# Kernel tuning notes

Measured on AMD Instinct MI355X. Metric: run time of the kernel, lower is better.

## Reference

```python
import jax, jax.numpy as jnp
import numpy as np

CONTEXT_LENGTHS = [1, 3, 5, 7]
PADS = [(f - 1) // 2 for f in CONTEXT_LENGTHS]  # p(f) for odd f
B, H, L, DK = 2, 8, 1024, 64
C = H * DK  # conv channels = d_k * n_heads


def _conv1d(x, w, b, pad):
    # x: (b, C, L), w: (C, C, f), b: (C,) -- torch Conv1d semantics
    y = jax.lax.conv_general_dilated(
        x, w, window_strides=(1,), padding=[(pad, pad)],
        dimension_numbers=("NCH", "OIH", "NCH"))
    return y + b[None, :, None]


def _plane(a, w, b, pad, out_len):
    # Faithful to: conv(a.reshape(b, h*d_k, -1)).reshape(b, h, -1, d_k)[:, :, :out_len, :]
    bsz, h, l, d = a.shape
    y = _conv1d(a.reshape(bsz, h * d, l), w, b, pad)
    return y.reshape(bsz, h, -1, d)[:, :, :out_len, :]


def setup_inputs() -> dict:
    key = jax.random.key(0)
    ks = jax.random.split(key, 12)
    inp = {
        "Q": jax.random.normal(ks[0], (B, H, L, DK), jnp.float32),
        "K": jax.random.normal(ks[1], (B, H, L, DK), jnp.float32),
        "V": jax.random.normal(ks[2], (B, H, L, DK), jnp.float32),
        # causal mask: True = masked
        "attn_mask": jnp.broadcast_to(
            jnp.triu(jnp.ones((L, L), jnp.bool_), k=1), (B, H, L, L)),
    }
    for i, f in enumerate(CONTEXT_LENGTHS):
        scale = 1.0 / np.sqrt(C * f)
        inp[f"conv_w{i}"] = jax.random.normal(ks[3 + i], (C, C, f), jnp.float32) * scale
        inp[f"conv_b{i}"] = jax.random.normal(ks[7 + i], (C,), jnp.float32) * scale
    return inp


def reference(Q, K, V, attn_mask,
              conv_w0, conv_b0, conv_w1, conv_b1,
              conv_w2, conv_b2, conv_w3, conv_b3):
    ws = [conv_w0, conv_w1, conv_w2, conv_w3]
    bs = [conv_b0, conv_b1, conv_b2, conv_b3]
    b, h, l, d_k = Q.shape
    l_k = K.shape[2]
    p = len(CONTEXT_LENGTHS)
    Q_l = [_plane(Q, ws[i], bs[i], PADS[i], l) for i in range(p)]
    K_l = [_plane(K, ws[i], bs[i], PADS[i], l_k) for i in range(p)]
    # replicate torch.cat(dim=0).reshape(b, h, p, l, d) exactly (row-major)
    Q_p = jnp.concatenate(Q_l, axis=0).reshape(b, h, p, l, d_k)
    K_p = jnp.concatenate(K_l, axis=0).reshape(b, h, p, l_k, d_k)
    scores = jnp.einsum("bhpqd,bhpkd->bhpqk", Q_p, K_p) / np.sqrt(d_k).astype(np.float32)
    scores = jnp.where(attn_mask[:, :, None, :, :], jnp.float32(-1e9), scores)
    attn = jax.nn.softmax(scores, axis=-1)
    attn = jnp.max(attn, axis=2)  # max over planes -> (b,h,q,k)
    context = jnp.einsum("bhqk,bhkd->bhqd", attn, V)
    return (context, attn)
```

## Files before the change

kernel.cpp:

```cpp
#include <hip/hip_runtime.h>
#include <math.h>

#define C_CH 512
#define L_SEQ 1024
#define DK 64
#define NP 4
#define SC2 0.1803368801111f

typedef __attribute__((ext_vector_type(8))) short short8;
typedef __attribute__((ext_vector_type(4))) float f32x4;

__device__ __forceinline__ unsigned short f2bf(float f) {
    union { float f; unsigned u; } v; v.f = f;
    unsigned u = v.u;
    u += 0x7FFFu + ((u >> 16) & 1u);
    return (unsigned short)(u >> 16);
}

__device__ __forceinline__ void unpack_group(int G, int& qt, int& kt0, int& kt1,
                                             int& j, int& ng) {
    int q = 15, cum = 0, jj = 0;
    for (; q >= 0; q--) {
        int g = (q + 4) >> 2;
        if (G < cum + g) { jj = G - cum; break; }
        cum += g;
    }
    qt = q;
    ng = (q + 4) >> 2;
    j = jj;
    int n = q + 1;
    kt0 = (jj * n) / ng;
    kt1 = ((jj + 1) * n) / ng;
}

__global__ __launch_bounds__(256)
void prep_w_kernel(const float* __restrict__ w0, const float* __restrict__ w1,
                   const float* __restrict__ w2, const float* __restrict__ w3,
                   unsigned short* __restrict__ Wb) {
    int tg = blockIdx.y;
    int plane, t;
    if (tg < 1)      { plane = 0; t = tg; }
    else if (tg < 4) { plane = 1; t = tg - 1; }
    else if (tg < 9) { plane = 2; t = tg - 4; }
    else             { plane = 3; t = tg - 9; }
    const float* W = (plane == 0) ? w0 : (plane == 1) ? w1 : (plane == 2) ? w2 : w3;
    const int f = (plane == 0) ? 1 : (plane == 1) ? 3 : (plane == 2) ? 5 : 7;

    int co = blockIdx.x * 32 + (threadIdx.x >> 3);
    int c8 = threadIdx.x & 7;
    for (int it = 0; it < 8; it++) {
        int ci = c8 * 8 + it * 64;
        unsigned short o[8];
#pragma unroll
        for (int jj = 0; jj < 8; jj++)
            o[jj] = f2bf(W[(size_t)(co * C_CH + ci + jj) * f + t]);
        *(short8*)&Wb[((size_t)tg * C_CH + co) * C_CH + ci] = *(short8*)o;
    }
}

__global__ __launch_bounds__(256)
void prep_x_kernel(const float* __restrict__ Qin, const float* __restrict__ Kin,
                   unsigned short* __restrict__ Xt) {
    int tb = blockIdx.z;
    int tensor = tb >> 1, b = tb & 1;
    const float* X = (tensor ? Kin : Qin) + (size_t)b * C_CH * L_SEQ;
    unsigned short* O = Xt + (size_t)tb * 1032 * C_CH;

    int pos0 = blockIdx.x * 64;
    int ci0  = blockIdx.y * 64;
    int tid = threadIdx.x;

    __shared__ float tile[64][65];
    int tx = tid & 15, ty = tid >> 4;
#pragma unroll
    for (int rr = 0; rr < 4; rr++) {
        int ci_l = ty + rr * 16;
        float4 v = *(const float4*)&X[(size_t)(ci0 + ci_l) * L_SEQ + pos0 + tx * 4];
        tile[tx * 4 + 0][ci_l] = v.x;
        tile[tx * 4 + 1][ci_l] = v.y;
        tile[tx * 4 + 2][ci_l] = v.z;
        tile[tx * 4 + 3][ci_l] = v.w;
    }
    __syncthreads();
#pragma unroll
    for (int pp = 0; pp < 2; pp++) {
        int pos_l = (tid >> 3) + pp * 32;
        int cg = (tid & 7) * 8;
        unsigned short o[8];
#pragma unroll
        for (int jj = 0; jj < 8; jj++) o[jj] = f2bf(tile[pos_l][cg + jj]);
        *(short8*)&O[(size_t)(pos0 + pos_l + 4) * C_CH + ci0 + cg] = *(short8*)o;
    }
    if (blockIdx.x == 0) {
        int r = tid >> 6, cc = tid & 63;
        O[(size_t)r * C_CH + ci0 + cc] = 0;
    }
    if (blockIdx.x == 15) {
        int r = tid >> 6, cc = tid & 63;
        O[(size_t)(1028 + r) * C_CH + ci0 + cc] = 0;
    }
}

__global__ __launch_bounds__(256)
void conv_mfma_kernel(const unsigned short* __restrict__ Xt,
                      const unsigned short* __restrict__ Wb,
                      const float* __restrict__ b0, const float* __restrict__ b1,
                      const float* __restrict__ b2, const float* __restrict__ b3,
                      unsigned short* __restrict__ Qp, unsigned short* __restrict__ Kp) {
    const int fs[4]   = {1, 3, 5, 7};
    const int toff[4] = {0, 1, 4, 9};
    int id = blockIdx.x;
    int plane, rel;
    if (id < 128)      { plane = 0; rel = id; }
    else if (id < 256) { plane = 1; rel = id - 128; }
    else if (id < 384) { plane = 3; rel = id - 256; }
    else               { plane = 2; rel = id - 384; }
    int co0  = (rel & 3) * 128;
    int pos0 = ((rel >> 2) & 7) * 128;
    int tb   = rel >> 5;
    int tensor = tb >> 1, b = tb & 1;
    const int f   = fs[plane];
    const int pad = (f - 1) >> 1;
    const int n   = f * 16;
    const float* bias = (plane == 0) ? b0 : (plane == 1) ? b1 : (plane == 2) ? b2 : b3;
    unsigned short* Out = tensor ? Kp : Qp;
    const unsigned short* Xbase = Xt + (size_t)tb * 1032 * C_CH;

    __shared__ __align__(16) unsigned short As[2][4096];
    __shared__ __align__(16) unsigned short Bs[2][4096];

    int tid  = threadIdx.x;
    int w    = tid >> 6;
    int lane = tid & 63;
    int l15  = lane & 15;
    int quad = lane >> 4;
    int wm = (w & 1) * 64;
    int wn = (w >> 1) * 64;
    int rowL = tid >> 2;
    int cS   = tid & 3;

    int woff[2];
#pragma unroll
    for (int rep = 0; rep < 2; rep++) {
        int r = rowL + rep * 64;
        int line = r >> 1;
        int sl = (((r & 1) << 2) | cS) ^ (line & 7);
        woff[rep] = line * 64 + sl * 8;
    }
    int aoff[4], boff[4];
#pragma unroll
    for (int mi = 0; mi < 4; mi++) {
        int r = wm + mi * 16 + l15;
        int line = r >> 1;
        aoff[mi] = line * 64 + ((((r & 1) << 2) | quad) ^ (line & 7)) * 8;
        int r2 = wn + mi * 16 + l15;
        int line2 = r2 >> 1;
        boff[mi] = line2 * 64 + ((((r2 & 1) << 2) | quad) ^ (line2 & 7)) * 8;
    }

    f32x4 acc[4][4];
#pragma unroll
    for (int mi = 0; mi < 4; mi++)
#pragma unroll
        for (int ni = 0; ni < 4; ni++) acc[mi][ni] = (f32x4){0.f, 0.f, 0.f, 0.f};

    short8 pA[2], pB[2];
    {
        const unsigned short* Wsl = Wb + ((size_t)toff[plane] * C_CH + co0) * C_CH;
        const unsigned short* Xsl = Xbase + (size_t)(pos0 - pad + 4) * C_CH;
#pragma unroll
        for (int rep = 0; rep < 2; rep++) {
            int r = rowL + rep * 64;
            pA[rep] = *(const short8*)&Wsl[(size_t)r * C_CH + cS * 8];
            pB[rep] = *(const short8*)&Xsl[(size_t)r * C_CH + cS * 8];
        }
    }

    for (int it = 0; it < n; it++) {
        int cur = it & 1;
        *(short8*)&As[cur][woff[0]] = pA[0];
        *(short8*)&As[cur][woff[1]] = pA[1];
        *(short8*)&Bs[cur][woff[0]] = pB[0];
        *(short8*)&Bs[cur][woff[1]] = pB[1];
        __syncthreads();

        if (it + 1 < n) {
            int t = (it + 1) >> 4, cc = (it + 1) & 15;
            const unsigned short* Wsl =
                Wb + ((size_t)(toff[plane] + t) * C_CH + co0) * C_CH + cc * 32;
            const unsigned short* Xsl =
                Xbase + (size_t)(pos0 + t - pad + 4) * C_CH + cc * 32;
#pragma unroll
            for (int rep = 0; rep < 2; rep++) {
                int r = rowL + rep * 64;
                pA[rep] = *(const short8*)&Wsl[(size_t)r * C_CH + cS * 8];
                pB[rep] = *(const short8*)&Xsl[(size_t)r * C_CH + cS * 8];
            }
        }

        short8 af[4], bf[4];
#pragma unroll
        for (int mi = 0; mi < 4; mi++) af[mi] = *(const short8*)&As[cur][aoff[mi]];
#pragma unroll
        for (int ni = 0; ni < 4; ni++) bf[ni] = *(const short8*)&Bs[cur][boff[ni]];
#pragma unroll
        for (int mi = 0; mi < 4; mi++)
#pragma unroll
            for (int ni = 0; ni < 4; ni++)
                acc[mi][ni] = __builtin_amdgcn_mfma_f32_16x16x32_bf16(
                    af[mi], bf[ni], acc[mi][ni], 0, 0, 0);
    }

#pragma unroll
    for (int mi = 0; mi < 4; mi++)
#pragma unroll
        for (int r = 0; r < 4; r++) {
            int co = co0 + wm + mi * 16 + quad * 4 + r;
            int h = co >> 6, cl = co & 63;
            float bv = bias[co];
            size_t sbase = (size_t)((b * 8 + h) * NP + plane) * L_SEQ * DK;
#pragma unroll
            for (int ni = 0; ni < 4; ni++) {
                int pos = pos0 + wn + ni * 16 + l15;
                int l = cl * 16 + (pos >> 6);
                int d = pos & 63;
                Out[sbase + (size_t)l * DK + d] = f2bf(acc[mi][ni][r] + bv);
            }
        }
}

__global__ __launch_bounds__(256)
void attn_stats_kernel(const unsigned short* __restrict__ Qb,
                       const unsigned short* __restrict__ Kb,
                       float* __restrict__ pl) {
    int qt, kt0, kt1, j, ng;
    unpack_group(blockIdx.x, qt, kt0, kt1, j, ng);
    int bh = blockIdx.y;
    int tid = threadIdx.x;
    int q0 = qt * 64;

    int b2 = bh >> 3, h2 = bh & 7;
    int plane  = b2 * 2 + (h2 >> 2);
    int b_orig = (h2 >> 1) & 1;
    int h_base = (h2 & 1) * 4;
    int w = tid >> 6, lane = tid & 63, l15 = lane & 15, quad = lane >> 4;

    const unsigned short* kbase[NP];
    short8 qa[NP][2];
#pragma unroll
    for (int p = 0; p < NP; p++) {
        size_t slice = (size_t)((b_orig * 8 + h_base + p) * NP + plane);
        kbase[p] = Kb + slice * L_SEQ * DK;
        const unsigned short* qrow =
            Qb + (slice * L_SEQ + (size_t)(q0 + w * 16 + l15)) * DK + quad * 8;
        qa[p][0] = *(const short8*)(qrow);
        qa[p][1] = *(const short8*)(qrow + 32);
    }

    float l[NP][4];
#pragma unroll
    for (int p = 0; p < NP; p++)
        for (int r = 0; r < 4; r++) l[p][r] = 0.f;

    for (int kt = kt0; kt < kt1; kt++) {
        int k0 = kt * 64;
        bool diag = (kt == qt);
#pragma unroll
        for (int p = 0; p < NP; p++) {
            f32x4 c[4];
#pragma unroll
            for (int s = 0; s < 4; s++) {
                const unsigned short* kr =
                    kbase[p] + (size_t)(k0 + s * 16 + l15) * DK + quad * 8;
                short8 kb0 = *(const short8*)(kr);
                short8 kb1 = *(const short8*)(kr + 32);
                f32x4 acc = {0.f, 0.f, 0.f, 0.f};
                acc = __builtin_amdgcn_mfma_f32_16x16x32_bf16(qa[p][0], kb0, acc, 0, 0, 0);
                acc = __builtin_amdgcn_mfma_f32_16x16x32_bf16(qa[p][1], kb1, acc, 0, 0, 0);
                c[s] = acc;
            }
#pragma unroll
            for (int r = 0; r < 4; r++) {
                int row_local = quad * 4 + r + w * 16;
#pragma unroll
                for (int s = 0; s < 4; s++) {
                    float x = c[s][r] * SC2;
                    if (diag && (s * 16 + l15 > row_local)) x = -1e30f;
                    l[p][r] += exp2f(x);
                }
            }
        }
    }

    size_t base = ((size_t)(bh * 16 + qt) * 4 + j) * 256;
#pragma unroll
    for (int p = 0; p < NP; p++)
#pragma unroll
        for (int r = 0; r < 4; r++) {
            float ll = l[p][r];
            ll += __shfl_xor(ll, 1);
            ll += __shfl_xor(ll, 2);
            ll += __shfl_xor(ll, 4);
            ll += __shfl_xor(ll, 8);
            if (l15 == 0)
                pl[base + p * 64 + (w * 16 + quad * 4 + r)] = ll;
        }
}

__global__ __launch_bounds__(256)
void attn_combine_kernel(const float* __restrict__ pl,
                         float* __restrict__ fstats,
                         float* __restrict__ out_attn) {
    int qt = blockIdx.x, bh = blockIdx.y;
    int tid = threadIdx.x;
    int ng = (qt + 4) >> 2;
    size_t sb = (size_t)(bh * 16 + qt) * 4 * 256;

    float l = 0.f;
    for (int g = 0; g < ng; g++)
        l += pl[sb + (size_t)g * 256 + tid];
    fstats[(size_t)(bh * 16 + qt) * 256 + tid] = __log2f(l);

    int r = tid >> 2;
    float4 z = make_float4(0.f, 0.f, 0.f, 0.f);
    int kz = (qt + 1) * 64;
    size_t abase = ((size_t)bh * L_SEQ + qt * 64 + r) * L_SEQ;
    for (int k = kz + (tid & 3) * 4; k < L_SEQ; k += 16)
        *(float4*)&out_attn[abase + k] = z;
}

__global__ __launch_bounds__(256)
void attn_apply_kernel(const unsigned short* __restrict__ Qb,
                       const unsigned short* __restrict__ Kb,
                       const float* __restrict__ V,
                       const float* __restrict__ fstats,
                       float* __restrict__ pctx, float* __restrict__ out_attn) {
    int qt, kt0, kt1, j, ng;
    unpack_group(blockIdx.x, qt, kt0, kt1, j, ng);
    int bh = blockIdx.y;
    int tid = threadIdx.x;
    int q0 = qt * 64;

    int b2 = bh >> 3, h2 = bh & 7;
    int plane  = b2 * 2 + (h2 >> 2);
    int b_orig = (h2 >> 1) & 1;
    int h_base = (h2 & 1) * 4;
    int w = tid >> 6, lane = tid & 63, l15 = lane & 15, quad = lane >> 4;

    __shared__ float zsm[NP * 64];
    __shared__ __align__(16) unsigned short ast[64 * 80];
    __shared__ __align__(16) unsigned short vts[2][64 * 80];

    zsm[tid] = fstats[(size_t)(bh * 16 + qt) * 256 + tid];

    const unsigned short* kbase[NP];
    short8 qa[NP][2];
#pragma unroll
    for (int p = 0; p < NP; p++) {
        size_t slice = (size_t)((b_orig * 8 + h_base + p) * NP + plane);
        kbase[p] = Kb + slice * L_SEQ * DK;
        const unsigned short* qrow =
            Qb + (slice * L_SEQ + (size_t)(q0 + w * 16 + l15)) * DK + quad * 8;
        qa[p][0] = *(const short8*)(qrow);
        qa[p][1] = *(const short8*)(qrow + 32);
    }

    f32x4 ctxc[4];
#pragma unroll
    for (int ds = 0; ds < 4; ds++) ctxc[ds] = (f32x4){0.f, 0.f, 0.f, 0.f};

    for (int kt = kt0; kt < kt1; kt++) {
        int k0 = kt * 64;
        bool diag = (kt == qt);
        unsigned short* vb = vts[kt & 1];

        {
            int kl = tid >> 2, db = (tid & 3) * 16;
            const float* vr = V + ((size_t)bh * L_SEQ + k0 + kl) * DK + db;
            float vv[16];
            *(float4*)&vv[0]  = *(const float4*)(vr);
            *(float4*)&vv[4]  = *(const float4*)(vr + 4);
            *(float4*)&vv[8]  = *(const float4*)(vr + 8);
            *(float4*)&vv[12] = *(const float4*)(vr + 12);
#pragma unroll
            for (int jj = 0; jj < 16; jj++)
                vb[(db + jj) * 80 + kl] = f2bf(vv[jj]);
        }
        __syncthreads();

        float run[4][4];
#pragma unroll
        for (int s = 0; s < 4; s++)
            for (int r = 0; r < 4; r++) run[s][r] = -1e30f;

#pragma unroll
        for (int p = 0; p < NP; p++) {
            f32x4 c[4];
#pragma unroll
            for (int s = 0; s < 4; s++) {
                const unsigned short* kr =
                    kbase[p] + (size_t)(k0 + s * 16 + l15) * DK + quad * 8;
                short8 kb0 = *(const short8*)(kr);
                short8 kb1 = *(const short8*)(kr + 32);
                f32x4 acc = {0.f, 0.f, 0.f, 0.f};
                acc = __builtin_amdgcn_mfma_f32_16x16x32_bf16(qa[p][0], kb0, acc, 0, 0, 0);
                acc = __builtin_amdgcn_mfma_f32_16x16x32_bf16(qa[p][1], kb1, acc, 0, 0, 0);
                c[s] = acc;
            }
#pragma unroll
            for (int r = 0; r < 4; r++) {
                float zp = zsm[p * 64 + (quad * 4 + r + w * 16)];
#pragma unroll
                for (int s = 0; s < 4; s++)
                    run[s][r] = fmaxf(run[s][r], c[s][r] * SC2 - zp);
            }
        }

#pragma unroll
        for (int s = 0; s < 4; s++)
#pragma unroll
            for (int r = 0; r < 4; r++) {
                int qloc = w * 16 + quad * 4 + r;
                bool masked = diag && (s * 16 + l15 > qloc);
                float a = masked ? 0.f : exp2f(run[s][r]);
                out_attn[((size_t)bh * L_SEQ + q0 + qloc) * L_SEQ + k0 + s * 16 + l15] = a;
                ast[qloc * 80 + s * 16 + l15] = f2bf(a);
            }

        short8 af0 = *(const short8*)&ast[(w * 16 + l15) * 80 + quad * 8];
        short8 af1 = *(const short8*)&ast[(w * 16 + l15) * 80 + 32 + quad * 8];
#pragma unroll
        for (int ds = 0; ds < 4; ds++) {
            short8 bf0 = *(const short8*)&vb[(ds * 16 + l15) * 80 + quad * 8];
            short8 bf1 = *(const short8*)&vb[(ds * 16 + l15) * 80 + 32 + quad * 8];
            ctxc[ds] = __builtin_amdgcn_mfma_f32_16x16x32_bf16(af0, bf0, ctxc[ds], 0, 0, 0);
            ctxc[ds] = __builtin_amdgcn_mfma_f32_16x16x32_bf16(af1, bf1, ctxc[ds], 0, 0, 0);
        }
    }

    size_t pbase = ((size_t)(bh * 16 + qt) * 4 + j) * 4096;
#pragma unroll
    for (int ds = 0; ds < 4; ds++)
#pragma unroll
        for (int r = 0; r < 4; r++) {
            int qloc = w * 16 + quad * 4 + r;
            pctx[pbase + (size_t)qloc * 64 + ds * 16 + l15] = ctxc[ds][r];
        }
}

__global__ __launch_bounds__(256)
void ctx_reduce_kernel(const float* __restrict__ pctx, float* __restrict__ out_ctx) {
    int qt = blockIdx.x, bh = blockIdx.y;
    int tid = threadIdx.x;
    int ng = (qt + 4) >> 2;
    size_t base = (size_t)(bh * 16 + qt) * 4 * 4096;
    int row = tid >> 2, c = (tid & 3) * 16;
    size_t off = (size_t)row * 64 + c;

    float4 a0 = *(const float4*)&pctx[base + off];
    float4 a1 = *(const float4*)&pctx[base + off + 4];
    float4 a2 = *(const float4*)&pctx[base + off + 8];
    float4 a3 = *(const float4*)&pctx[base + off + 12];
    for (int g = 1; g < ng; g++) {
        size_t gb = base + (size_t)g * 4096 + off;
        float4 b0 = *(const float4*)&pctx[gb];
        float4 b1 = *(const float4*)&pctx[gb + 4];
        float4 b2 = *(const float4*)&pctx[gb + 8];
        float4 b3 = *(const float4*)&pctx[gb + 12];
        a0.x += b0.x; a0.y += b0.y; a0.z += b0.z; a0.w += b0.w;
        a1.x += b1.x; a1.y += b1.y; a1.z += b1.z; a1.w += b1.w;
        a2.x += b2.x; a2.y += b2.y; a2.z += b2.z; a2.w += b2.w;
        a3.x += b3.x; a3.y += b3.y; a3.z += b3.z; a3.w += b3.w;
    }
    size_t ob = ((size_t)bh * L_SEQ + qt * 64 + row) * DK + c;
    *(float4*)&out_ctx[ob]      = a0;
    *(float4*)&out_ctx[ob + 4]  = a1;
    *(float4*)&out_ctx[ob + 8]  = a2;
    *(float4*)&out_ctx[ob + 12] = a3;
}

extern "C" void kernel_launch(void* const* d_in, const int* in_sizes, int n_in,
                              void* d_out, int out_size, void* d_ws, size_t ws_size,
                              hipStream_t stream) {
    const float* Q  = (const float*)d_in[0];
    const float* K  = (const float*)d_in[1];
    const float* V  = (const float*)d_in[2];
    const float* w0 = (const float*)d_in[4];
    const float* b0 = (const float*)d_in[5];
    const float* w1 = (const float*)d_in[6];
    const float* b1 = (const float*)d_in[7];
    const float* w2 = (const float*)d_in[8];
    const float* b2 = (const float*)d_in[9];
    const float* w3 = (const float*)d_in[10];
    const float* b3 = (const float*)d_in[11];

    char* ws = (char*)d_ws;
    unsigned short* Wb = (unsigned short*)(ws);
    unsigned short* Xt = (unsigned short*)(ws + 8388608);
    unsigned short* Qp = (unsigned short*)(ws + 12615680);
    unsigned short* Kp = (unsigned short*)(ws + 21004288);
    float* pctx        = (float*)(ws + 29392896);
    float* pl     = (float*)(ws + 8388608);
    float* fstats = (float*)(ws + 8388608 + 1048576);

    float* out_ctx  = (float*)d_out;
    float* out_attn = out_ctx + 1048576;

    prep_w_kernel<<<dim3(16, 16), 256, 0, stream>>>(w0, w1, w2, w3, Wb);
    prep_x_kernel<<<dim3(16, 8, 4), 256, 0, stream>>>(Q, K, Xt);
    conv_mfma_kernel<<<dim3(512), 256, 0, stream>>>(Xt, Wb, b0, b1, b2, b3, Qp, Kp);
    attn_stats_kernel<<<dim3(40, 16), 256, 0, stream>>>(Qp, Kp, pl);
    attn_combine_kernel<<<dim3(16, 16), 256, 0, stream>>>(pl, fstats, out_attn);
    attn_apply_kernel<<<dim3(40, 16), 256, 0, stream>>>(Qp, Kp, V, fstats,
                                                        pctx, out_attn);
    ctx_reduce_kernel<<<dim3(16, 16), 256, 0, stream>>>(pctx, out_ctx);
}
```

Baseline: 355.4 us.

## Halve conv tile width, stage output via LDS, fold combine kernel into neighbors

The conv GEMM tile shrinks from 128x128 to 128x64 positions, doubling the grid to 1024 blocks for better CU fill. The epilogue is staged through shared memory so each thread writes 16-byte coalesced rows instead of scattered 2-byte stores. The separate combine kernel is removed: the stats kernel gets extra blocks that zero the masked part of the attention output, and the apply kernel sums the partial row sums and takes the log itself. This saves one launch and more parallelism in exchange for less reuse per conv tile and some redundant reductions.

```diff
diff --git a/kernel.cpp b/kernel.cpp
--- a/kernel.cpp
+++ b/kernel.cpp
@@ -110,14 +110,11 @@
     const int fs[4]   = {1, 3, 5, 7};
     const int toff[4] = {0, 1, 4, 9};
     int id = blockIdx.x;
-    int plane, rel;
-    if (id < 128)      { plane = 0; rel = id; }
-    else if (id < 256) { plane = 1; rel = id - 128; }
-    else if (id < 384) { plane = 3; rel = id - 256; }
-    else               { plane = 2; rel = id - 384; }
+    int plane = (id < 256) ? 0 : (id < 512) ? 1 : (id < 768) ? 3 : 2;
+    int rel = id & 255;
     int co0  = (rel & 3) * 128;
-    int pos0 = ((rel >> 2) & 7) * 128;
-    int tb   = rel >> 5;
+    int pos0 = ((rel >> 2) & 15) * 64;
+    int tb   = rel >> 6;
     int tensor = tb >> 1, b = tb & 1;
     const int f   = fs[plane];
     const int pad = (f - 1) >> 1;
@@ -127,7 +124,7 @@
     const unsigned short* Xbase = Xt + (size_t)tb * 1032 * C_CH;
 
     __shared__ __align__(16) unsigned short As[2][4096];
-    __shared__ __align__(16) unsigned short Bs[2][4096];
+    __shared__ __align__(16) unsigned short Bs[2][2048];
 
     int tid  = threadIdx.x;
     int w    = tid >> 6;
@@ -135,53 +132,54 @@
     int l15  = lane & 15;
     int quad = lane >> 4;
     int wm = (w & 1) * 64;
-    int wn = (w >> 1) * 64;
-    int rowL = tid >> 2;
-    int cS   = tid & 3;
-
-    int woff[2];
+    int wn = (w >> 1) * 32;
+
+    int rA0 = tid >> 2, sA = tid & 3;
+    int woffA[2], woffB;
 #pragma unroll
     for (int rep = 0; rep < 2; rep++) {
-        int r = rowL + rep * 64;
+        int r = rA0 + rep * 64;
         int line = r >> 1;
-        int sl = (((r & 1) << 2) | cS) ^ (line & 7);
-        woff[rep] = line * 64 + sl * 8;
-    }
-    int aoff[4], boff[4];
+        woffA[rep] = line * 64 + (((((r & 1) << 2) | sA)) ^ (line & 7)) * 8;
+    }
+    {
+        int line = rA0 >> 1;
+        woffB = line * 64 + (((((rA0 & 1) << 2) | sA)) ^ (line & 7)) * 8;
+    }
+    int aoff[4], boff[2];
 #pragma unroll
     for (int mi = 0; mi < 4; mi++) {
         int r = wm + mi * 16 + l15;
         int line = r >> 1;
         aoff[mi] = line * 64 + ((((r & 1) << 2) | quad) ^ (line & 7)) * 8;
-        int r2 = wn + mi * 16 + l15;
-        int line2 = r2 >> 1;
-        boff[mi] = line2 * 64 + ((((r2 & 1) << 2) | quad) ^ (line2 & 7)) * 8;
-    }
-
-    f32x4 acc[4][4];
+    }
+#pragma unroll
+    for (int ni = 0; ni < 2; ni++) {
+        int r = wn + ni * 16 + l15;
+        int line = r >> 1;
+        boff[ni] = line * 64 + ((((r & 1) << 2) | quad) ^ (line & 7)) * 8;
+    }
+
+    f32x4 acc[4][2];
 #pragma unroll
     for (int mi = 0; mi < 4; mi++)
 #pragma unroll
-        for (int ni = 0; ni < 4; ni++) acc[mi][ni] = (f32x4){0.f, 0.f, 0.f, 0.f};
-
-    short8 pA[2], pB[2];
+        for (int ni = 0; ni < 2; ni++) acc[mi][ni] = (f32x4){0.f, 0.f, 0.f, 0.f};
+
+    short8 pA[2], pB;
     {
         const unsigned short* Wsl = Wb + ((size_t)toff[plane] * C_CH + co0) * C_CH;
         const unsigned short* Xsl = Xbase + (size_t)(pos0 - pad + 4) * C_CH;
-#pragma unroll
-        for (int rep = 0; rep < 2; rep++) {
-            int r = rowL + rep * 64;
-            pA[rep] = *(const short8*)&Wsl[(size_t)r * C_CH + cS * 8];
-            pB[rep] = *(const short8*)&Xsl[(size_t)r * C_CH + cS * 8];
-        }
+        pA[0] = *(const short8*)&Wsl[(size_t)rA0 * C_CH + sA * 8];
+        pA[1] = *(const short8*)&Wsl[(size_t)(rA0 + 64) * C_CH + sA * 8];
+        pB    = *(const short8*)&Xsl[(size_t)rA0 * C_CH + sA * 8];
     }
 
     for (int it = 0; it < n; it++) {
         int cur = it & 1;
-        *(short8*)&As[cur][woff[0]] = pA[0];
-        *(short8*)&As[cur][woff[1]] = pA[1];
-        *(short8*)&Bs[cur][woff[0]] = pB[0];
-        *(short8*)&Bs[cur][woff[1]] = pB[1];
+        *(short8*)&As[cur][woffA[0]] = pA[0];
+        *(short8*)&As[cur][woffA[1]] = pA[1];
+        *(short8*)&Bs[cur][woffB]    = pB;
         __syncthreads();
 
         if (it + 1 < n) {
@@ -190,53 +188,76 @@
                 Wb + ((size_t)(toff[plane] + t) * C_CH + co0) * C_CH + cc * 32;
             const unsigned short* Xsl =
                 Xbase + (size_t)(pos0 + t - pad + 4) * C_CH + cc * 32;
-#pragma unroll
-            for (int rep = 0; rep < 2; rep++) {
-                int r = rowL + rep * 64;
-                pA[rep] = *(const short8*)&Wsl[(size_t)r * C_CH + cS * 8];
-                pB[rep] = *(const short8*)&Xsl[(size_t)r * C_CH + cS * 8];
-            }
-        }
-
-        short8 af[4], bf[4];
+            pA[0] = *(const short8*)&Wsl[(size_t)rA0 * C_CH + sA * 8];
+            pA[1] = *(const short8*)&Wsl[(size_t)(rA0 + 64) * C_CH + sA * 8];
+            pB    = *(const short8*)&Xsl[(size_t)rA0 * C_CH + sA * 8];
+        }
+
+        short8 af[4], bf[2];
 #pragma unroll
         for (int mi = 0; mi < 4; mi++) af[mi] = *(const short8*)&As[cur][aoff[mi]];
 #pragma unroll
-        for (int ni = 0; ni < 4; ni++) bf[ni] = *(const short8*)&Bs[cur][boff[ni]];
+        for (int ni = 0; ni < 2; ni++) bf[ni] = *(const short8*)&Bs[cur][boff[ni]];
 #pragma unroll
         for (int mi = 0; mi < 4; mi++)
 #pragma unroll
-            for (int ni = 0; ni < 4; ni++)
+            for (int ni = 0; ni < 2; ni++)
                 acc[mi][ni] = __builtin_amdgcn_mfma_f32_16x16x32_bf16(
                     af[mi], bf[ni], acc[mi][ni], 0, 0, 0);
     }
 
+    __syncthreads();
+    unsigned short* Cs = &As[0][0];
 #pragma unroll
     for (int mi = 0; mi < 4; mi++)
 #pragma unroll
         for (int r = 0; r < 4; r++) {
-            int co = co0 + wm + mi * 16 + quad * 4 + r;
-            int h = co >> 6, cl = co & 63;
-            float bv = bias[co];
-            size_t sbase = (size_t)((b * 8 + h) * NP + plane) * L_SEQ * DK;
-#pragma unroll
-            for (int ni = 0; ni < 4; ni++) {
-                int pos = pos0 + wn + ni * 16 + l15;
-                int l = cl * 16 + (pos >> 6);
-                int d = pos & 63;
-                Out[sbase + (size_t)l * DK + d] = f2bf(acc[mi][ni][r] + bv);
-            }
-        }
+            int co_l = wm + mi * 16 + quad * 4 + r;
+            float bv = bias[co0 + co_l];
+#pragma unroll
+            for (int ni = 0; ni < 2; ni++)
+                Cs[co_l * 64 + wn + ni * 16 + l15] = f2bf(acc[mi][ni][r] + bv);
+        }
+    __syncthreads();
+    {
+        int co_l = tid >> 1, half = tid & 1;
+        int co = co0 + co_l;
+        int h = co >> 6, cl = co & 63;
+        int l = cl * 16 + (pos0 >> 6);
+        size_t obase =
+            ((size_t)((b * 8 + h) * NP + plane) * L_SEQ + l) * DK + half * 32;
+#pragma unroll
+        for (int k = 0; k < 4; k++)
+            *(short8*)&Out[obase + k * 8] =
+                *(const short8*)&Cs[co_l * 64 + half * 32 + k * 8];
+    }
 }
 
 __global__ __launch_bounds__(256)
 void attn_stats_kernel(const unsigned short* __restrict__ Qb,
                        const unsigned short* __restrict__ Kb,
-                       float* __restrict__ pl) {
+                       float* __restrict__ pl, float* __restrict__ out_attn) {
+    int tid = threadIdx.x;
+    int bh = blockIdx.y;
+
+    if (blockIdx.x >= 40) {
+        int z = blockIdx.x - 40;
+        int qts[2] = {z, 15 - z};
+        float4 zv = make_float4(0.f, 0.f, 0.f, 0.f);
+#pragma unroll
+        for (int i = 0; i < 2; i++) {
+            int qt = qts[i];
+            int kz = (qt + 1) * 64;
+            int r = tid >> 2;
+            size_t abase = ((size_t)bh * L_SEQ + qt * 64 + r) * L_SEQ;
+            for (int k = kz + (tid & 3) * 4; k < L_SEQ; k += 16)
+                *(float4*)&out_attn[abase + k] = zv;
+        }
+        return;
+    }
+
     int qt, kt0, kt1, j, ng;
     unpack_group(blockIdx.x, qt, kt0, kt1, j, ng);
-    int bh = blockIdx.y;
-    int tid = threadIdx.x;
     int q0 = qt * 64;
 
     int b2 = bh >> 3, h2 = bh & 7;
@@ -308,32 +329,10 @@
 }
 
 __global__ __launch_bounds__(256)
-void attn_combine_kernel(const float* __restrict__ pl,
-                         float* __restrict__ fstats,
-                         float* __restrict__ out_attn) {
-    int qt = blockIdx.x, bh = blockIdx.y;
-    int tid = threadIdx.x;
-    int ng = (qt + 4) >> 2;
-    size_t sb = (size_t)(bh * 16 + qt) * 4 * 256;
-
-    float l = 0.f;
-    for (int g = 0; g < ng; g++)
-        l += pl[sb + (size_t)g * 256 + tid];
-    fstats[(size_t)(bh * 16 + qt) * 256 + tid] = __log2f(l);
-
-    int r = tid >> 2;
-    float4 z = make_float4(0.f, 0.f, 0.f, 0.f);
-    int kz = (qt + 1) * 64;
-    size_t abase = ((size_t)bh * L_SEQ + qt * 64 + r) * L_SEQ;
-    for (int k = kz + (tid & 3) * 4; k < L_SEQ; k += 16)
-        *(float4*)&out_attn[abase + k] = z;
-}
-
-__global__ __launch_bounds__(256)
 void attn_apply_kernel(const unsigned short* __restrict__ Qb,
                        const unsigned short* __restrict__ Kb,
                        const float* __restrict__ V,
-                       const float* __restrict__ fstats,
+                       const float* __restrict__ pl,
                        float* __restrict__ pctx, float* __restrict__ out_attn) {
     int qt, kt0, kt1, j, ng;
     unpack_group(blockIdx.x, qt, kt0, kt1, j, ng);
@@ -351,7 +350,13 @@
     __shared__ __align__(16) unsigned short ast[64 * 80];
     __shared__ __align__(16) unsigned short vts[2][64 * 80];
 
-    zsm[tid] = fstats[(size_t)(bh * 16 + qt) * 256 + tid];
+    {
+        size_t sb = ((size_t)(bh * 16 + qt) * 4) * 256 + tid;
+        float lsum = pl[sb];
+        for (int g = 1; g < ng; g++)
+            lsum += pl[sb + (size_t)g * 256];
+        zsm[tid] = __log2f(lsum);
+    }
 
     const unsigned short* kbase[NP];
     short8 qa[NP][2];
@@ -500,18 +505,15 @@
     unsigned short* Qp = (unsigned short*)(ws + 12615680);
     unsigned short* Kp = (unsigned short*)(ws + 21004288);
     float* pctx        = (float*)(ws + 29392896);
-    float* pl     = (float*)(ws + 8388608);
-    float* fstats = (float*)(ws + 8388608 + 1048576);
+    float* pl = (float*)(ws);
 
     float* out_ctx  = (float*)d_out;
     float* out_attn = out_ctx + 1048576;
 
     prep_w_kernel<<<dim3(16, 16), 256, 0, stream>>>(w0, w1, w2, w3, Wb);
     prep_x_kernel<<<dim3(16, 8, 4), 256, 0, stream>>>(Q, K, Xt);
-    conv_mfma_kernel<<<dim3(512), 256, 0, stream>>>(Xt, Wb, b0, b1, b2, b3, Qp, Kp);
-    attn_stats_kernel<<<dim3(40, 16), 256, 0, stream>>>(Qp, Kp, pl);
-    attn_combine_kernel<<<dim3(16, 16), 256, 0, stream>>>(pl, fstats, out_attn);
-    attn_apply_kernel<<<dim3(40, 16), 256, 0, stream>>>(Qp, Kp, V, fstats,
-                                                        pctx, out_attn);
+    conv_mfma_kernel<<<dim3(1024), 256, 0, stream>>>(Xt, Wb, b0, b1, b2, b3, Qp, Kp);
+    attn_stats_kernel<<<dim3(48, 16), 256, 0, stream>>>(Qp, Kp, pl, out_attn);
+    attn_apply_kernel<<<dim3(40, 16), 256, 0, stream>>>(Qp, Kp, V, pl, pctx, out_attn);
     ctx_reduce_kernel<<<dim3(16, 16), 256, 0, stream>>>(pctx, out_ctx);
 }
```

Result: faster. 341.3 us (-4.0%).
